# Performance work log

Hardware: AMD Instinct MI355X
Metric: run time of the kernel (lower is better)

Reference implementation:

```python
import jax, jax.numpy as jnp
import numpy as np

L, D, H, DFF, P, B = 10, 512, 8, 1536, 16, 1024
DK = D // H
SQRT_DK = float(np.sqrt(DK))

# board geometry constants (square index -> rank/file/diag)
_pos = np.arange(64)
FILES = _pos % 8
RANKS = _pos // 8
DIAGS = RANKS + FILES
ADIAGS = RANKS - FILES + 7
RIDX = np.clip(RANKS[:, None] - RANKS[None, :], -7, 7) + 7  # [64,64]
FIDX = np.clip(FILES[:, None] - FILES[None, :], -7, 7) + 7  # [64,64]


def setup_inputs() -> dict:
    key = jax.random.key(0)
    ks = iter(jax.random.split(key, 40))
    n = lambda shape, s=0.02: (jax.random.normal(next(ks), shape, jnp.float32) * s)
    inp = {
        'x': jax.random.normal(next(ks), (B, 64, P), jnp.float32),
        'emb_W': n((P, D)), 'emb_b': jnp.zeros((D,), jnp.float32),
        'cls': n((1, 1, D)), 'abs_pos': n((1, 64, D)),
        'file_tab': n((8, D)), 'rank_tab': n((8, D)),
        'diag_tab': n((15, D)), 'anti_tab': n((15, D)),
        'rel_bias': n((L, 15, 15, H)),
        'Wq': n((L, D, D)), 'bq': jnp.zeros((L, D)),
        'Wk': n((L, D, D)), 'bk': jnp.zeros((L, D)),
        'Wv': n((L, D, D)), 'bv': jnp.zeros((L, D)),
        'Wo': n((L, D, D)), 'bo': jnp.zeros((L, D)),
        'ln1_g': jnp.ones((L, D)), 'ln1_b': jnp.zeros((L, D)),
        'ln2_g': jnp.ones((L, D)), 'ln2_b': jnp.zeros((L, D)),
        'W1': n((L, D, 2 * DFF)), 'b1': jnp.zeros((L, 2 * DFF)),
        'W2': n((L, DFF, D)), 'b2': jnp.zeros((L, D)),
        'fln_g': jnp.ones((D,)), 'fln_b': jnp.zeros((D,)),
        'pol_W': n((D, 72)), 'pol_b': jnp.zeros((72,)),
        'v1_W': n((D, D // 2)), 'v1_b': jnp.zeros((D // 2,)),
        'v2_W': n((D // 2, 128)), 'v2_b': jnp.zeros((128,)),
        'v3_W': n((128, 1)), 'v3_b': jnp.zeros((1,)),
    }
    return inp


def _ln(x, g, b):
    m = x.mean(-1, keepdims=True)
    v = ((x - m) ** 2).mean(-1, keepdims=True)
    return (x - m) * jax.lax.rsqrt(v + 1e-5) * g + b


def _gelu(x):
    return jax.nn.gelu(x, approximate=False)  # torch F.gelu default (erf)


def reference(x, emb_W, emb_b, cls, abs_pos, file_tab, rank_tab, diag_tab, anti_tab,
              rel_bias, Wq, bq, Wk, bk, Wv, bv, Wo, bo, ln1_g, ln1_b, ln2_g, ln2_b,
              W1, b1, W2, b2, fln_g, fln_b, pol_W, pol_b,
              v1_W, v1_b, v2_W, v2_b, v3_W, v3_b):
    Bn = x.shape[0]
    # per-square embedding + chess positional encoding
    emb = x @ emb_W + emb_b                                   # [B,64,D]
    pe = abs_pos + file_tab[FILES] + rank_tab[RANKS] + diag_tab[DIAGS] + anti_tab[ADIAGS]
    t = emb + pe
    t = jnp.concatenate([jnp.broadcast_to(cls, (Bn, 1, D)), t], axis=1)  # [B,65,D]
    for i in range(L):
        h = _ln(t, ln1_g[i], ln1_b[i])
        q = (h @ Wq[i] + bq[i]).reshape(Bn, 65, H, DK).transpose(0, 2, 1, 3)
        k = (h @ Wk[i] + bk[i]).reshape(Bn, 65, H, DK).transpose(0, 2, 1, 3)
        v = (h @ Wv[i] + bv[i]).reshape(Bn, 65, H, DK).transpose(0, 2, 1, 3)
        scores = jnp.einsum('bhqd,bhkd->bhqk', q, k) / SQRT_DK
        bias = rel_bias[i][RIDX, FIDX]                        # [64,64,H]
        bias = jnp.pad(bias.transpose(2, 0, 1), ((0, 0), (1, 0), (1, 0)))  # zero bias for CLS
        scores = scores + bias[None]
        a = jax.nn.softmax(scores, axis=-1)
        ctx = jnp.einsum('bhqk,bhkd->bhqd', a, v).transpose(0, 2, 1, 3).reshape(Bn, 65, D)
        t = t + (ctx @ Wo[i] + bo[i])
        h = _ln(t, ln2_g[i], ln2_b[i])
        p = h @ W1[i] + b1[i]
        x1, x2 = jnp.split(p, 2, axis=-1)
        t = t + (_gelu(x1) * x2) @ W2[i] + b2[i]
    t = _ln(t, fln_g, fln_b)
    policy = (t[:, 1:] @ pol_W + pol_b).reshape(Bn, -1)       # [B,4608]
    vh = t[:, 0]                                              # CLS token
    value = jnp.tanh(_gelu(_gelu(vh @ v1_W + v1_b) @ v2_W + v2_b) @ v3_W + v3_b)  # [B,1]
    return policy, value
```

## Files before the change

kernel.cpp:

```cpp
#include <hip/hip_runtime.h>
#include <hip/hip_bf16.h>
#include <math.h>


typedef short short8 __attribute__((ext_vector_type(8)));
typedef float f32x4 __attribute__((ext_vector_type(4)));

#define NLAYER 10
#define DMODEL 512
#define NHEAD 8
#define BATCH 1024
#define SEQ 65

#define WT_QKV   0L
#define WT_WO    7864320L
#define WT_W1    10485760L
#define WT_W2    26214400L
#define WT_BQKV  34078720L
#define WT_BO    34094080L
#define WT_B1    34099200L
#define WT_B2    34129920L
#define WT_TOTAL 34135040L

__device__ __forceinline__ float bf2f(ushort u){ return __uint_as_float(((unsigned)u)<<16); }
__device__ __forceinline__ ushort f2bf(float f){
  unsigned u = __float_as_uint(f);
  unsigned r = (u + 0x7fffu + ((u>>16)&1u)) >> 16;
  return (ushort)r;
}
__device__ __forceinline__ float gelu_exact(float x){
  return 0.5f*x*(1.0f+erff(x*0.70710678118654752440f));
}
__device__ __forceinline__ void gl16(ushort* lds, const ushort* g){
  __builtin_amdgcn_global_load_lds(
      (const unsigned int __attribute__((address_space(1)))*)g,
      (unsigned int __attribute__((address_space(3)))*)lds,
      16, 0, 0);
}

__global__ void prep_qkv(const float* __restrict__ Wq, const float* __restrict__ Wk,
                         const float* __restrict__ Wv, ushort* __restrict__ wT)
{
  long idx = (long)blockIdx.x*256 + threadIdx.x;
  if(idx >= 7864320L) return;
  int l = (int)(idx/786432L);
  long r = idx - (long)l*786432L;
  int n = (int)(r>>9), k = (int)(r&511);
  float v;
  if(n<512)       v = Wq[(long)l*262144 + (long)k*512 + n];
  else if(n<1024) v = Wk[(long)l*262144 + (long)k*512 + (n-512)];
  else            v = Wv[(long)l*262144 + (long)k*512 + (n-1024)];
  wT[WT_QKV + idx] = f2bf(v);
}
__global__ void prep_wo(const float* __restrict__ Wo, ushort* __restrict__ wT)
{
  long idx = (long)blockIdx.x*256 + threadIdx.x;
  if(idx >= 2621440L) return;
  int l = (int)(idx/262144L);
  long r = idx - (long)l*262144L;
  int n = (int)(r>>9), k = (int)(r&511);
  wT[WT_WO + idx] = f2bf(Wo[(long)l*262144 + (long)k*512 + n]);
}
__global__ void prep_w1(const float* __restrict__ W1, ushort* __restrict__ wT)
{
  long idx = (long)blockIdx.x*256 + threadIdx.x;
  if(idx >= 15728640L) return;
  int l = (int)(idx/1572864L);
  long r = idx - (long)l*1572864L;
  int n = (int)(r>>9), k = (int)(r&511);
  int j = n>>1;
  int src = (n&1) ? 1536+j : j;
  wT[WT_W1 + idx] = f2bf(W1[(long)l*1572864 + (long)k*3072 + src]);
}
__global__ void prep_w2(const float* __restrict__ W2, ushort* __restrict__ wT)
{
  long idx = (long)blockIdx.x*256 + threadIdx.x;
  if(idx >= 7864320L) return;
  int l = (int)(idx/786432L);
  long r = idx - (long)l*786432L;
  int n = (int)(r/1536), k = (int)(r - (long)n*1536);
  wT[WT_W2 + idx] = f2bf(W2[(long)l*786432 + (long)k*512 + n]);
}
__global__ void prep_bias(const float* __restrict__ bq, const float* __restrict__ bk,
                          const float* __restrict__ bv, const float* __restrict__ bo,
                          const float* __restrict__ b1, const float* __restrict__ b2,
                          ushort* __restrict__ wT)
{
  int idx = blockIdx.x*256 + threadIdx.x;
  if(idx >= 56320) return;
  long o = WT_BQKV + idx;
  float v;
  if(o < WT_BO){
    int i = idx;
    int l = i/1536, n = i - l*1536;
    if(n<512) v=bq[l*512+n]; else if(n<1024) v=bk[l*512+n-512]; else v=bv[l*512+n-1024];
  } else if(o < WT_B1){
    int i = (int)(o - WT_BO);
    v = bo[i];
  } else if(o < WT_B2){
    int i = (int)(o - WT_B1);
    int l = i/3072, n = i - l*3072;
    int j=n>>1; int src=(n&1)?1536+j:j;
    v = b1[l*3072+src];
  } else {
    int i = (int)(o - WT_B2);
    v = b2[i];
  }
  wT[o] = f2bf(v);
}

__global__ __launch_bounds__(64) void embed_kernel(
    const float* __restrict__ x, const float* __restrict__ emb_W,
    const float* __restrict__ emb_b, const float* __restrict__ cls,
    const float* __restrict__ abs_pos, const float* __restrict__ file_tab,
    const float* __restrict__ rank_tab, const float* __restrict__ diag_tab,
    const float* __restrict__ anti_tab, float* __restrict__ t, long xoff)
{
  long tok = blockIdx.x;
  int lane = threadIdx.x;
  long b = tok/SEQ;
  int s = (int)(tok - b*SEQ);
  float* out = t + tok*DMODEL;
  if(s==0){
    #pragma unroll
    for(int j=0;j<8;j++){ int d=lane*8+j; out[d]=cls[d]; }
    return;
  }
  int p = s-1;
  int f = p&7, r = p>>3;
  int dg = r+f, ad = r-f+7;
  float xv[16];
  #pragma unroll
  for(int k=0;k<16;k++) xv[k]=x[xoff + (b*64+p)*16+k];
  #pragma unroll
  for(int j=0;j<8;j++){
    int d = lane*8+j;
    float acc = emb_b[d] + abs_pos[p*512+d] + file_tab[f*512+d]
              + rank_tab[r*512+d] + diag_tab[dg*512+d] + anti_tab[ad*512+d];
    #pragma unroll
    for(int k=0;k<16;k++) acc += xv[k]*emb_W[k*512+d];
    out[d]=acc;
  }
}

__global__ __launch_bounds__(64) void ln_kernel(const float* __restrict__ t, ushort* __restrict__ h,
                                                const float* __restrict__ g, const float* __restrict__ b,
                                                long goff)
{
  long tok = blockIdx.x;
  int lane = threadIdx.x;
  const float* row = t + tok*DMODEL;
  float4 v0 = *reinterpret_cast<const float4*>(row + lane*8);
  float4 v1 = *reinterpret_cast<const float4*>(row + lane*8 + 4);
  float x[8] = {v0.x,v0.y,v0.z,v0.w,v1.x,v1.y,v1.z,v1.w};
  float s=0.f, ss=0.f;
  #pragma unroll
  for(int j=0;j<8;j++){ s+=x[j]; ss+=x[j]*x[j]; }
  #pragma unroll
  for(int off=32;off>=1;off>>=1){ s+=__shfl_down(s,off); ss+=__shfl_down(ss,off); }
  s=__shfl(s,0); ss=__shfl(ss,0);
  float mean = s*(1.0f/512.0f);
  float var  = ss*(1.0f/512.0f) - mean*mean;
  float rs = rsqrtf(fmaxf(var,0.0f) + 1e-5f);
  #pragma unroll
  for(int j=0;j<8;j++){
    int d=lane*8+j;
    h[tok*DMODEL+d] = f2bf((x[j]-mean)*rs*g[goff+d] + b[goff+d]);
  }
}

template<int EPI>
__global__ __launch_bounds__(256,2) void gemm_bt(
    const ushort* __restrict__ A, long lda,
    const ushort* __restrict__ BT,
    const ushort* __restrict__ bias,
    ushort* __restrict__ Cb, float* __restrict__ Cf,
    long ldc, int K)
{
  __shared__ __align__(16) ushort As[128*32];
  __shared__ __align__(16) ushort Bs[128*32];
  const int tid = threadIdx.x;
  const int w = tid>>6, lane = tid&63, q = lane>>4, lr = lane&15;
  const int wm = (w>>1)*64, wn = (w&1)*64;
  const long mBase = (long)blockIdx.y*128, nBase = (long)blockIdx.x*128;

  f32x4 acc[4][4];
  #pragma unroll
  for(int i=0;i<4;i++)
    #pragma unroll
    for(int j=0;j<4;j++) acc[i][j]=(f32x4)(0.0f);

  const int idx0=tid, idx1=tid+256;
  const int ar0=idx0>>2, ac0=(idx0&3)*8;
  const int ar1=idx1>>2, ac1=(idx1&3)*8;

  const ushort* gA0 = A  + (mBase+ar0)*lda     + ac0;
  const ushort* gA1 = A  + (mBase+ar1)*lda     + ac1;
  const ushort* gB0 = BT + (nBase+ar0)*(long)K + ac0;
  const ushort* gB1 = BT + (nBase+ar1)*(long)K + ac1;
  ushort* lA0 = As + idx0*8;
  ushort* lA1 = As + idx1*8;
  ushort* lB0 = Bs + idx0*8;
  ushort* lB1 = Bs + idx1*8;

  for(int k0=0;k0<K;k0+=32){
    __syncthreads();
    gl16(lA0, gA0 + k0);
    gl16(lA1, gA1 + k0);
    gl16(lB0, gB0 + k0);
    gl16(lB1, gB1 + k0);
    __syncthreads();
    short8 af[4], bfr[4];
    #pragma unroll
    for(int mt=0;mt<4;mt++) af[mt]=*reinterpret_cast<const short8*>(As + (wm+mt*16+lr)*32 + q*8);
    #pragma unroll
    for(int nt=0;nt<4;nt++) bfr[nt]=*reinterpret_cast<const short8*>(Bs + (wn+nt*16+lr)*32 + q*8);
    #pragma unroll
    for(int mt=0;mt<4;mt++)
      #pragma unroll
      for(int nt=0;nt<4;nt++)
        acc[mt][nt]=__builtin_amdgcn_mfma_f32_16x16x32_bf16(af[mt],bfr[nt],acc[mt][nt],0,0,0);
  }

  #pragma unroll
  for(int nt=0;nt<4;nt++){
    long n = nBase+wn+nt*16+lr;
    float bv = bf2f(bias[n]);
    #pragma unroll
    for(int mt=0;mt<4;mt++){
      #pragma unroll
      for(int r=0;r<4;r++){
        long m = mBase+wm+mt*16+q*4+r;
        float v = acc[mt][nt][r]+bv;
        if constexpr (EPI==0){
          Cb[m*ldc+n]=f2bf(v);
        } else if constexpr (EPI==1){
          Cf[m*ldc+n]+=v;
        } else {
          float partner = __shfl_xor(v,1);
          if(!(lane&1)) Cb[m*ldc + (n>>1)] = f2bf(gelu_exact(v)*partner);
        }
      }
    }
  }
}

__global__ __launch_bounds__(256) void attn_kernel(const ushort* __restrict__ qkv,
                                                   const float* __restrict__ rel_bias,
                                                   ushort* __restrict__ ctx, int layer)
{
  int bh = blockIdx.x;
  long b = bh>>3;
  int h = bh&7;
  __shared__ __align__(16) ushort Qb[80*72];
  __shared__ __align__(16) ushort Kb[80*72];
  __shared__ __align__(16) ushort Vt[64*104];
  __shared__ __align__(16) float  S [80*81];
  __shared__ __align__(16) ushort Pb[80*104];
  __shared__ float relb[225];
  const long tokBase = b*SEQ;
  const int tid = threadIdx.x;
  const int w = tid>>6, lane = tid&63, q = lane>>4, lr = lane&15;

  for(int idx=tid; idx<SEQ*8; idx+=256){
    int s = idx>>3, c8 = (idx&7)<<3;
    long base = (tokBase+s)*1536 + h*64 + c8;
    *reinterpret_cast<short8*>(&Qb[s*72 + c8]) = *reinterpret_cast<const short8*>(&qkv[base]);
    *reinterpret_cast<short8*>(&Kb[s*72 + c8]) = *reinterpret_cast<const short8*>(&qkv[base+512]);
    short8 v = *reinterpret_cast<const short8*>(&qkv[base+1024]);
    #pragma unroll
    for(int j=0;j<8;j++) Vt[(c8+j)*104 + s] = (ushort)v[j];
  }
  for(int idx=tid; idx<64*32; idx+=256){
    int d = idx>>5, s = 65+(idx&31);
    Vt[d*104 + s] = 0;
  }
  if(tid<225) relb[tid] = rel_bias[((long)layer*225 + tid)*8 + h];
  __syncthreads();

  for(int tt=w; tt<25; tt+=4){
    int mt = tt/5, nt = tt - mt*5;
    f32x4 acc = (f32x4)(0.0f);
    #pragma unroll
    for(int ks=0;ks<2;ks++){
      short8 af = *reinterpret_cast<const short8*>(&Qb[(mt*16+lr)*72 + ks*32 + q*8]);
      short8 bf = *reinterpret_cast<const short8*>(&Kb[(nt*16+lr)*72 + ks*32 + q*8]);
      acc = __builtin_amdgcn_mfma_f32_16x16x32_bf16(af, bf, acc, 0,0,0);
    }
    int col = nt*16 + lr;
    #pragma unroll
    for(int r=0;r<4;r++)
      S[(mt*16 + q*4 + r)*81 + col] = acc[r]*0.125f;
  }
  __syncthreads();

  if(tid < SEQ){
    int qi = tid;
    float* srow = S + qi*81;
    int pq = qi-1;
    float mx = -1e30f;
    for(int k=0;k<SEQ;k++){
      float s = srow[k];
      if(qi>0 && k>0){
        int pk = k-1;
        int ridx = (pq>>3)-(pk>>3)+7, fidx = (pq&7)-(pk&7)+7;
        s += relb[ridx*15+fidx];
      }
      srow[k] = s;
      mx = fmaxf(mx, s);
    }
    float sum = 0.f;
    for(int k=0;k<SEQ;k++){ float e = __expf(srow[k]-mx); srow[k]=e; sum+=e; }
    float inv = 1.0f/sum;
    ushort* prow = Pb + qi*104;
    for(int k=0;k<SEQ;k++) prow[k] = f2bf(srow[k]*inv);
    for(int k=SEQ;k<96;k++) prow[k] = 0;
  }
  __syncthreads();

  for(int tt=w; tt<20; tt+=4){
    int mt = tt>>2, nt = tt&3;
    f32x4 acc = (f32x4)(0.0f);
    #pragma unroll
    for(int ks=0;ks<3;ks++){
      short8 af = *reinterpret_cast<const short8*>(&Pb[(mt*16+lr)*104 + ks*32 + q*8]);
      short8 bf = *reinterpret_cast<const short8*>(&Vt[(nt*16+lr)*104 + ks*32 + q*8]);
      acc = __builtin_amdgcn_mfma_f32_16x16x32_bf16(af, bf, acc, 0,0,0);
    }
    int col = nt*16 + lr;
    #pragma unroll
    for(int r=0;r<4;r++){
      int row = mt*16 + q*4 + r;
      if(row < SEQ)
        ctx[(tokBase+row)*512 + h*64 + col] = f2bf(acc[r]);
    }
  }
}

__global__ __launch_bounds__(128) void policy_kernel(const ushort* __restrict__ h,
                                                     const float* __restrict__ pol_W,
                                                     const float* __restrict__ pol_b,
                                                     float* __restrict__ out, long b0)
{
  int bp = blockIdx.x;
  long bl = bp>>6;
  int p = bp&63;
  const ushort* hrow = h + (bl*SEQ + 1 + p)*DMODEL;
  __shared__ float hl[DMODEL];
  for(int d=threadIdx.x; d<DMODEL; d+=128) hl[d]=bf2f(hrow[d]);
  __syncthreads();
  int j = threadIdx.x;
  if(j<72){
    float acc = pol_b[j];
    for(int k=0;k<DMODEL;k++) acc += hl[k]*pol_W[k*72+j];
    out[(b0+bl)*4608 + (long)p*72 + j] = acc;
  }
}

__global__ __launch_bounds__(256) void value_kernel(const ushort* __restrict__ h,
                                                    const float* __restrict__ v1_W, const float* __restrict__ v1_b,
                                                    const float* __restrict__ v2_W, const float* __restrict__ v2_b,
                                                    const float* __restrict__ v3_W, const float* __restrict__ v3_b,
                                                    float* __restrict__ out, long b0)
{
  long bl = blockIdx.x;
  int tid = threadIdx.x;
  __shared__ float vh[512], a1[256], a2[128];
  const ushort* hrow = h + bl*SEQ*DMODEL;
  for(int d=tid; d<512; d+=256) vh[d]=bf2f(hrow[d]);
  __syncthreads();
  {
    float acc = v1_b[tid];
    for(int k=0;k<512;k++) acc += vh[k]*v1_W[k*256+tid];
    a1[tid]=gelu_exact(acc);
  }
  __syncthreads();
  if(tid<128){
    float acc = v2_b[tid];
    for(int k=0;k<256;k++) acc += a1[k]*v2_W[k*128+tid];
    a2[tid]=gelu_exact(acc);
  }
  __syncthreads();
  if(tid==0){
    float acc = v3_b[0];
    for(int k=0;k<128;k++) acc += a2[k]*v3_W[k];
    out[(long)BATCH*4608 + b0 + bl] = tanhf(acc);
  }
}

extern "C" void kernel_launch(void* const* d_in, const int* in_sizes, int n_in,
                              void* d_out, int out_size, void* d_ws, size_t ws_size,
                              hipStream_t stream)
{
  const float* x        = (const float*)d_in[0];
  const float* emb_W    = (const float*)d_in[1];
  const float* emb_b    = (const float*)d_in[2];
  const float* cls      = (const float*)d_in[3];
  const float* abs_pos  = (const float*)d_in[4];
  const float* file_tab = (const float*)d_in[5];
  const float* rank_tab = (const float*)d_in[6];
  const float* diag_tab = (const float*)d_in[7];
  const float* anti_tab = (const float*)d_in[8];
  const float* rel_bias = (const float*)d_in[9];
  const float* Wq  = (const float*)d_in[10];
  const float* bq  = (const float*)d_in[11];
  const float* Wk  = (const float*)d_in[12];
  const float* bk  = (const float*)d_in[13];
  const float* Wv  = (const float*)d_in[14];
  const float* bv  = (const float*)d_in[15];
  const float* Wo  = (const float*)d_in[16];
  const float* bo  = (const float*)d_in[17];
  const float* ln1_g = (const float*)d_in[18];
  const float* ln1_b = (const float*)d_in[19];
  const float* ln2_g = (const float*)d_in[20];
  const float* ln2_b = (const float*)d_in[21];
  const float* W1  = (const float*)d_in[22];
  const float* b1  = (const float*)d_in[23];
  const float* W2  = (const float*)d_in[24];
  const float* b2  = (const float*)d_in[25];
  const float* fln_g = (const float*)d_in[26];
  const float* fln_b = (const float*)d_in[27];
  const float* pol_W = (const float*)d_in[28];
  const float* pol_b = (const float*)d_in[29];
  const float* v1_W  = (const float*)d_in[30];
  const float* v1_b  = (const float*)d_in[31];
  const float* v2_W  = (const float*)d_in[32];
  const float* v2_b  = (const float*)d_in[33];
  const float* v3_W  = (const float*)d_in[34];
  const float* v3_b  = (const float*)d_in[35];
  float* out = (float*)d_out;

  int nchunk = 4;
  if(ws_size >= (size_t)477214720) nchunk = 1;
  else if(ws_size >= (size_t)272742400) nchunk = 2;
  const int bch = BATCH / nchunk;
  const long mch = (long)bch * SEQ;

  char* ws = (char*)d_ws;
  float*  t    = (float*)ws;  ws += (size_t)mch*DMODEL*4;
  ushort* h    = (ushort*)ws; ws += (size_t)mch*DMODEL*2;
  ushort* buf1 = (ushort*)ws; ws += (size_t)mch*1536*2;
  ushort* wT   = (ushort*)ws; ws += (size_t)WT_TOTAL*2;
  (void)ws_size; (void)in_sizes; (void)n_in; (void)out_size;

  prep_qkv<<<(7864320+255)/256,256,0,stream>>>(Wq,Wk,Wv,wT);
  prep_wo <<<(2621440+255)/256,256,0,stream>>>(Wo,wT);
  prep_w1 <<<(15728640+255)/256,256,0,stream>>>(W1,wT);
  prep_w2 <<<(7864320+255)/256,256,0,stream>>>(W2,wT);
  prep_bias<<<(56320+255)/256,256,0,stream>>>(bq,bk,bv,bo,b1,b2,wT);

  const int gy = (int)(mch/128);
  for(int c=0;c<nchunk;c++){
    long b0 = (long)c*bch;
    embed_kernel<<<(int)mch,64,0,stream>>>(x, emb_W, emb_b, cls, abs_pos,
                                      file_tab, rank_tab, diag_tab, anti_tab, t, b0*64*16);
    for(int l=0;l<NLAYER;l++){
      ln_kernel<<<(int)mch,64,0,stream>>>(t, h, ln1_g, ln1_b, l*512);
      gemm_bt<0><<<dim3(12,gy),256,0,stream>>>(h, 512, wT+WT_QKV+(long)l*786432,
                                                wT+WT_BQKV+l*1536, buf1, nullptr, 1536, 512);
      attn_kernel<<<bch*NHEAD,256,0,stream>>>(buf1, rel_bias, h, l);
      gemm_bt<1><<<dim3(4,gy),256,0,stream>>>(h, 512, wT+WT_WO+(long)l*262144,
                                               wT+WT_BO+l*512, nullptr, t, 512, 512);
      ln_kernel<<<(int)mch,64,0,stream>>>(t, h, ln2_g, ln2_b, l*512);
      gemm_bt<2><<<dim3(24,gy),256,0,stream>>>(h, 512, wT+WT_W1+(long)l*1572864,
                                                wT+WT_B1+l*3072, buf1, nullptr, 1536, 512);
      gemm_bt<1><<<dim3(4,gy),256,0,stream>>>(buf1, 1536, wT+WT_W2+(long)l*786432,
                                               wT+WT_B2+l*512, nullptr, t, 512, 1536);
    }
    ln_kernel<<<(int)mch,64,0,stream>>>(t, h, fln_g, fln_b, 0);
    policy_kernel<<<bch*64,128,0,stream>>>(h, pol_W, pol_b, out, b0);
    value_kernel<<<bch,256,0,stream>>>(h, v1_W, v1_b, v2_W, v2_b, v3_W, v3_b, out, b0);
  }
}
```

Before: 13.15 ms.

## Triple-buffer GEMM LDS loads with async prefetch; pack four rows per LayerNorm block

```diff
diff --git a/kernel.cpp b/kernel.cpp
--- a/kernel.cpp
+++ b/kernel.cpp
@@ -143,12 +143,12 @@
   }
 }
 
-__global__ __launch_bounds__(64) void ln_kernel(const float* __restrict__ t, ushort* __restrict__ h,
-                                                const float* __restrict__ g, const float* __restrict__ b,
-                                                long goff)
-{
-  long tok = blockIdx.x;
-  int lane = threadIdx.x;
+__global__ __launch_bounds__(256) void ln_kernel(const float* __restrict__ t, ushort* __restrict__ h,
+                                                 const float* __restrict__ g, const float* __restrict__ b,
+                                                 long goff)
+{
+  long tok = (long)blockIdx.x*4 + (threadIdx.x>>6);
+  int lane = threadIdx.x&63;
   const float* row = t + tok*DMODEL;
   float4 v0 = *reinterpret_cast<const float4*>(row + lane*8);
   float4 v1 = *reinterpret_cast<const float4*>(row + lane*8 + 4);
@@ -177,8 +177,8 @@
     ushort* __restrict__ Cb, float* __restrict__ Cf,
     long ldc, int K)
 {
-  __shared__ __align__(16) ushort As[128*32];
-  __shared__ __align__(16) ushort Bs[128*32];
+  __shared__ __align__(16) ushort LA[3][128*32];
+  __shared__ __align__(16) ushort LB[3][128*32];
   const int tid = threadIdx.x;
   const int w = tid>>6, lane = tid&63, q = lane>>4, lr = lane&15;
   const int wm = (w>>1)*64, wn = (w&1)*64;
@@ -198,18 +198,34 @@
   const ushort* gA1 = A  + (mBase+ar1)*lda     + ac1;
   const ushort* gB0 = BT + (nBase+ar0)*(long)K + ac0;
   const ushort* gB1 = BT + (nBase+ar1)*(long)K + ac1;
-  ushort* lA0 = As + idx0*8;
-  ushort* lA1 = As + idx1*8;
-  ushort* lB0 = Bs + idx0*8;
-  ushort* lB1 = Bs + idx1*8;
-
-  for(int k0=0;k0<K;k0+=32){
-    __syncthreads();
-    gl16(lA0, gA0 + k0);
-    gl16(lA1, gA1 + k0);
-    gl16(lB0, gB0 + k0);
-    gl16(lB1, gB1 + k0);
-    __syncthreads();
+
+  const int NT = K>>5;
+
+  #define STAGE(bf,kt) do{ int _k0=(kt)<<5;                 \
+      gl16(&LA[bf][idx0*8], gA0 + _k0);                     \
+      gl16(&LA[bf][idx1*8], gA1 + _k0);                     \
+      gl16(&LB[bf][idx0*8], gB0 + _k0);                     \
+      gl16(&LB[bf][idx1*8], gB1 + _k0); }while(0)
+
+  STAGE(0,0);
+  STAGE(1,1);
+
+  int c = 0;
+  for(int t=0;t<NT;t++){
+    if(t+2<NT){
+      int nb = c+2; if(nb>=3) nb-=3;
+      STAGE(nb, t+2);
+      asm volatile("s_waitcnt vmcnt(8)" ::: "memory");
+    } else if(t+1<NT){
+      asm volatile("s_waitcnt vmcnt(4)" ::: "memory");
+    } else {
+      asm volatile("s_waitcnt vmcnt(0)" ::: "memory");
+    }
+    __builtin_amdgcn_s_barrier();
+    __builtin_amdgcn_sched_barrier(0);
+
+    const ushort* As = LA[c];
+    const ushort* Bs = LB[c];
     short8 af[4], bfr[4];
     #pragma unroll
     for(int mt=0;mt<4;mt++) af[mt]=*reinterpret_cast<const short8*>(As + (wm+mt*16+lr)*32 + q*8);
@@ -220,7 +236,13 @@
       #pragma unroll
       for(int nt=0;nt<4;nt++)
         acc[mt][nt]=__builtin_amdgcn_mfma_f32_16x16x32_bf16(af[mt],bfr[nt],acc[mt][nt],0,0,0);
-  }
+
+    asm volatile("" ::: "memory");
+    __builtin_amdgcn_s_barrier();
+    __builtin_amdgcn_sched_barrier(0);
+    c = c+1; if(c>=3) c-=3;
+  }
+  #undef STAGE
 
   #pragma unroll
   for(int nt=0;nt<4;nt++){
@@ -450,24 +472,25 @@
   prep_bias<<<(56320+255)/256,256,0,stream>>>(bq,bk,bv,bo,b1,b2,wT);
 
   const int gy = (int)(mch/128);
+  const int lng = (int)(mch/4);
   for(int c=0;c<nchunk;c++){
     long b0 = (long)c*bch;
     embed_kernel<<<(int)mch,64,0,stream>>>(x, emb_W, emb_b, cls, abs_pos,
                                       file_tab, rank_tab, diag_tab, anti_tab, t, b0*64*16);
     for(int l=0;l<NLAYER;l++){
-      ln_kernel<<<(int)mch,64,0,stream>>>(t, h, ln1_g, ln1_b, l*512);
+      ln_kernel<<<lng,256,0,stream>>>(t, h, ln1_g, ln1_b, l*512);
       gemm_bt<0><<<dim3(12,gy),256,0,stream>>>(h, 512, wT+WT_QKV+(long)l*786432,
                                                 wT+WT_BQKV+l*1536, buf1, nullptr, 1536, 512);
       attn_kernel<<<bch*NHEAD,256,0,stream>>>(buf1, rel_bias, h, l);
       gemm_bt<1><<<dim3(4,gy),256,0,stream>>>(h, 512, wT+WT_WO+(long)l*262144,
                                                wT+WT_BO+l*512, nullptr, t, 512, 512);
-      ln_kernel<<<(int)mch,64,0,stream>>>(t, h, ln2_g, ln2_b, l*512);
+      ln_kernel<<<lng,256,0,stream>>>(t, h, ln2_g, ln2_b, l*512);
       gemm_bt<2><<<dim3(24,gy),256,0,stream>>>(h, 512, wT+WT_W1+(long)l*1572864,
                                                 wT+WT_B1+l*3072, buf1, nullptr, 1536, 512);
       gemm_bt<1><<<dim3(4,gy),256,0,stream>>>(buf1, 1536, wT+WT_W2+(long)l*786432,
                                                wT+WT_B2+l*512, nullptr, t, 512, 1536);
     }
-    ln_kernel<<<(int)mch,64,0,stream>>>(t, h, fln_g, fln_b, 0);
+    ln_kernel<<<lng,256,0,stream>>>(t, h, fln_g, fln_b, 0);
     policy_kernel<<<bch*64,128,0,stream>>>(h, pol_W, pol_b, out, b0);
     value_kernel<<<bch,256,0,stream>>>(h, v1_W, v1_b, v2_W, v2_b, v3_W, v3_b, out, b0);
   }
```

Result: slower. 13.58 ms (+3.2%).
